# Kernel optimization log

Measured on AMD Instinct MI355X. Metric: run time of the kernel, lower is better.

Reference implementation:

```python
import jax, jax.numpy as jnp
import numpy as np

N_NODES = 50000
N_EDGES = 1600000
IN_DIM, HID_DIM, OUT_DIM = 512, 256, 128
N_IDX = 8192


def _graph_conv(x, src, dst, W, b, n_nodes):
    # DGL GraphConv, norm='both': D_dst^{-1/2} A D_src^{-1/2} x W + b
    ones = jnp.ones(src.shape[0], dtype=x.dtype)
    deg_out = jax.ops.segment_sum(ones, src, num_segments=n_nodes)
    deg_in = jax.ops.segment_sum(ones, dst, num_segments=n_nodes)
    ns = jax.lax.rsqrt(jnp.maximum(deg_out, 1.0))  # source norm
    nd = jax.lax.rsqrt(jnp.maximum(deg_in, 1.0))   # dest norm
    msg = (x * ns[:, None])[src]                   # gather [E, F]
    agg = jax.ops.segment_sum(msg, dst, num_segments=n_nodes)
    return (agg * nd[:, None]) @ W + b


def _gcn(x, src, dst, W1, b1, W2, b2, n_nodes):
    h = jax.nn.relu(_graph_conv(x, src, dst, W1, b1, n_nodes))
    return _graph_conv(h, src, dst, W2, b2, n_nodes)


def setup_inputs() -> dict:
    key = jax.random.key(0)
    ks = jax.random.split(key, 16)
    d = {
        'raw1': jax.random.normal(ks[0], (N_NODES, IN_DIM), jnp.float32),
        'raw2': jax.random.normal(ks[1], (N_NODES, IN_DIM), jnp.float32),
        'src1': jax.random.randint(ks[2], (N_EDGES,), 0, N_NODES),
        'dst1': jax.random.randint(ks[3], (N_EDGES,), 0, N_NODES),
        'src2': jax.random.randint(ks[4], (N_EDGES,), 0, N_NODES),
        'dst2': jax.random.randint(ks[5], (N_EDGES,), 0, N_NODES),
        'index': jax.random.randint(ks[6], (N_IDX,), 0, N_NODES),
    }
    def lin(k, fi, fo):
        s = 1.0 / np.sqrt(fi)
        return jax.random.uniform(k, (fi, fo), jnp.float32, -s, s)
    d['e1_W1'] = lin(ks[7], IN_DIM, HID_DIM); d['e1_b1'] = jnp.zeros(HID_DIM, jnp.float32)
    d['e1_W2'] = lin(ks[8], HID_DIM, OUT_DIM); d['e1_b2'] = jnp.zeros(OUT_DIM, jnp.float32)
    d['e2_W1'] = lin(ks[9], IN_DIM, HID_DIM); d['e2_b1'] = jnp.zeros(HID_DIM, jnp.float32)
    d['e2_W2'] = lin(ks[10], HID_DIM, OUT_DIM); d['e2_b2'] = jnp.zeros(OUT_DIM, jnp.float32)
    return d


def reference(raw1, raw2, src1, dst1, src2, dst2, index,
              e1_W1, e1_b1, e1_W2, e1_b2, e2_W1, e2_b1, e2_W2, e2_b2):
    n = raw1.shape[0]
    c1 = _gcn(raw1, src1, dst1, e1_W1, e1_b1, e1_W2, e1_b2, n)[index]
    c2 = _gcn(raw2, src2, dst2, e2_W1, e2_b1, e2_W2, e2_b2, n)[index]
    # F.normalize(dim=1), eps=1e-12
    c1 = c1 / jnp.maximum(jnp.linalg.norm(c1, axis=1, keepdims=True), 1e-12)
    c2 = c2 / jnp.maximum(jnp.linalg.norm(c2, axis=1, keepdims=True), 1e-12)
    z1 = c1 @ c1.T
    z2 = c2 @ c2.T
    z3 = c1 @ c2.T
    z3 = (z3 + z3.T) * 0.5
    z = (z1 + z2 + z3) * (1.0 / 3.0)
    return jnp.triu(z)
```

## Files before the change

kernel.cpp:

```cpp
#include <hip/hip_runtime.h>
#include <hip/hip_bf16.h>

using u16 = unsigned short;
using u32 = unsigned int;

typedef __attribute__((ext_vector_type(8))) short short8;
typedef __attribute__((ext_vector_type(4))) float f32x4;

__device__ __forceinline__ u16 f2bf_u16(float f) {
    __hip_bfloat16 h = __float2bfloat16(f);
    return __builtin_bit_cast(u16, h);
}
__device__ __forceinline__ float bfu(u32 u) { return __uint_as_float(u << 16); }

static constexpr int NN = 50000;
static constexpr int NE = 1600000;
static constexpr int NIDX = 8192;
static constexpr int NRANGE = 8;
static constexpr int RN = NN / NRANGE;
static constexpr int HCH = 16;
static constexpr int NK = NN * NRANGE;
static constexpr int SAB = (NK + 4095) / 4096;
static constexpr int CAPB = 262144;
static constexpr int PEB = 8192;
static constexpr int PGX = (NE + PEB - 1) / PEB;
static constexpr int CVB = 640;
static constexpr int PSTG = 1536;
static constexpr int ZLB = 64 * 63 / 2;
static constexpr int ZHB = ZLB / 2;
static constexpr int ZUB = 64 * 65 / 2;
static constexpr int AGB = NN / 4;
static constexpr int MT = (NN + 127) / 128;
static constexpr int SCX = 256;


__global__ __launch_bounds__(256)
void partition_kernel(const int* __restrict__ s1, const int* __restrict__ d1,
                      const int* __restrict__ s2, const int* __restrict__ d2,
                      int* __restrict__ bcur, u32* __restrict__ ebuf_d, u16* __restrict__ ebuf_s,
                      const float* __restrict__ W1a, const float* __restrict__ W1b,
                      const float* __restrict__ W2a, const float* __restrict__ W2b,
                      u16* __restrict__ W1t, u16* __restrict__ W2t) {
    if (blockIdx.x >= PGX) {
        int o = (blockIdx.x - PGX) + CVB * blockIdx.y;
        int idx = o * 256 + threadIdx.x;
        if (idx < 131072) {
            int k = idx >> 8, n = idx & 255;
            W1t[(size_t)n * 512 + k] = f2bf_u16(W1a[idx]);
        } else if (idx < 262144) {
            int j = idx - 131072;
            int k = j >> 8, n = j & 255;
            W1t[(size_t)131072 + (size_t)n * 512 + k] = f2bf_u16(W1b[j]);
        } else if (idx < 294912) {
            int j = idx - 262144;
            int k = j >> 7, n = j & 127;
            W2t[(size_t)n * 256 + k] = f2bf_u16(W2a[j]);
        } else if (idx < 327680) {
            int j = idx - 294912;
            int k = j >> 7, n = j & 127;
            W2t[(size_t)32768 + (size_t)n * 256 + k] = f2bf_u16(W2b[j]);
        }
        return;
    }
    __shared__ u32 stage_d[8][PSTG];
    __shared__ u16 stage_s[8][PSTG];
    __shared__ int cnt_d[8], cnt_s[8], base_d[8], base_s[8];
    int enc = blockIdx.y;
    const int* s = enc ? s2 : s1;
    const int* d = enc ? d2 : d1;
    if (threadIdx.x < 8) { cnt_d[threadIdx.x] = 0; cnt_s[threadIdx.x] = 0; }
    __syncthreads();
    int* bc_d = bcur + enc * 16;
    int* bc_s = bcur + enc * 16 + 8;
    u32* bd = ebuf_d + (size_t)enc * 8 * CAPB;
    u16* bs = ebuf_s + (size_t)enc * 8 * CAPB;
    int e0 = blockIdx.x * PEB;
    int e1 = min(e0 + PEB, NE);
    for (int e = e0 + threadIdx.x * 4; e < e1; e += 1024) {
        int4 sv = *(const int4*)(s + e);
        int4 dv = *(const int4*)(d + e);
        #pragma unroll
        for (int j = 0; j < 4; ++j) {
            int src = j == 0 ? sv.x : j == 1 ? sv.y : j == 2 ? sv.z : sv.w;
            int dst = j == 0 ? dv.x : j == 1 ? dv.y : j == 2 ? dv.z : dv.w;
            int rd = dst / RN;
            u32 entry = (u32)src | ((u32)(dst - rd * RN) << 16);
            int slot = atomicAdd(&cnt_d[rd], 1);
            if (slot < PSTG) stage_d[rd][slot] = entry;
            else { int gp = atomicAdd(&bc_d[rd], 1); bd[(size_t)rd * CAPB + gp] = entry; }
            int rs = src / RN;
            int slot2 = atomicAdd(&cnt_s[rs], 1);
            if (slot2 < PSTG) stage_s[rs][slot2] = (u16)(src - rs * RN);
            else { int gp = atomicAdd(&bc_s[rs], 1); bs[(size_t)rs * CAPB + gp] = (u16)(src - rs * RN); }
        }
    }
    __syncthreads();
    if (threadIdx.x < 8) {
        int b = threadIdx.x;
        base_d[b] = atomicAdd(&bc_d[b], min(cnt_d[b], PSTG));
        base_s[b] = atomicAdd(&bc_s[b], min(cnt_s[b], PSTG));
    }
    __syncthreads();
    #pragma unroll
    for (int b = 0; b < 8; ++b) {
        int nb = min(cnt_d[b], PSTG);
        for (int i = threadIdx.x; i < nb; i += 256)
            bd[(size_t)b * CAPB + base_d[b] + i] = stage_d[b][i];
        int ns = min(cnt_s[b], PSTG);
        for (int i = threadIdx.x; i < ns; i += 256)
            bs[(size_t)b * CAPB + base_s[b] + i] = stage_s[b][i];
    }
}


__global__ __launch_bounds__(256)
void bhist_kernel(const u32* __restrict__ ebuf_d, const u16* __restrict__ ebuf_s,
                  const int* __restrict__ bcur,
                  u32* __restrict__ partial2, u32* __restrict__ partial_out) {
    __shared__ u32 sh[RN * 2];
    int stripe = blockIdx.x & 7, chunk = blockIdx.x >> 3;
    int enc = blockIdx.y & 1, type = blockIdx.y >> 1;
    if (type == 0) {
        for (int i = threadIdx.x; i < RN * 2; i += 256) sh[i] = 0;
        __syncthreads();
        int size = bcur[enc * 16 + stripe];
        int cs = (size + HCH - 1) / HCH;
        int lo = chunk * cs, hi = min(lo + cs, size);
        const u32* b = ebuf_d + ((size_t)enc * 8 + stripe) * CAPB;
        for (int i = lo + threadIdx.x; i < hi; i += 256) {
            u32 e = b[i];
            u32 idx = (e >> 16) * 8 + (e & 0xffffu) / RN;
            atomicAdd(&sh[idx >> 2], 1u << ((idx & 3) * 8));
        }
        __syncthreads();
        u32* p2 = partial2 + ((size_t)enc * HCH + chunk) * (NN * 2) + stripe * (RN * 2);
        for (int i = threadIdx.x; i < RN * 2; i += 256) p2[i] = sh[i];
    } else {
        for (int i = threadIdx.x; i < RN / 2; i += 256) sh[i] = 0;
        __syncthreads();
        int size = bcur[enc * 16 + 8 + stripe];
        int cs = (size + HCH - 1) / HCH;
        int lo = chunk * cs, hi = min(lo + cs, size);
        const u16* b = ebuf_s + ((size_t)enc * 8 + stripe) * CAPB;
        for (int i = lo + threadIdx.x; i < hi; i += 256) {
            u32 sl = b[i];
            atomicAdd(&sh[sl >> 1], 1u << ((sl & 1) * 16));
        }
        __syncthreads();
        u32* po = partial_out + ((size_t)enc * HCH + chunk) * (NN / 2) + stripe * (RN / 2);
        for (int i = threadIdx.x; i < RN / 2; i += 256) po[i] = sh[i];
    }
}

__global__ void reduce_hist_kernel(const u32* __restrict__ partial2,
                                   const u32* __restrict__ partial_out,
                                   int* __restrict__ deg2, float* __restrict__ norms) {
    int i = blockIdx.x * blockDim.x + threadIdx.x;
    if (i >= 2 * NN) return;
    int enc = i / NN;
    int dst = i - enc * NN;
    int cnt[8];
    #pragma unroll
    for (int r = 0; r < 8; ++r) cnt[r] = 0;
    for (int c = 0; c < HCH; ++c) {
        const u32* p = partial2 + ((size_t)enc * HCH + c) * (NN * 2) + dst * 2;
        u32 w0 = p[0], w1 = p[1];
        cnt[0] += w0 & 0xff; cnt[1] += (w0 >> 8) & 0xff; cnt[2] += (w0 >> 16) & 0xff; cnt[3] += w0 >> 24;
        cnt[4] += w1 & 0xff; cnt[5] += (w1 >> 8) & 0xff; cnt[6] += (w1 >> 16) & 0xff; cnt[7] += w1 >> 24;
    }
    int* dp = deg2 + (size_t)enc * NK + dst * 8;
    int din = 0;
    #pragma unroll
    for (int r = 0; r < 8; ++r) { dp[r] = cnt[r]; din += cnt[r]; }
    norms[(enc * 2 + 1) * NN + dst] = rsqrtf(fmaxf((float)din, 1.f));
    int dout = 0;
    for (int c = 0; c < HCH; ++c) {
        u32 w = partial_out[((size_t)enc * HCH + c) * (NN / 2) + (dst >> 1)];
        dout += (w >> ((dst & 1) * 16)) & 0xffff;
    }
    norms[(enc * 2 + 0) * NN + dst] = rsqrtf(fmaxf((float)dout, 1.f));
}


__global__ __launch_bounds__(1024)
void scanA_kernel(const int* __restrict__ deg2, int* __restrict__ rp2_all, int* __restrict__ tot) {
    int enc = blockIdx.y;
    const int* deg = deg2 + (size_t)enc * NK;
    int* rp = rp2_all + (size_t)enc * (NK + 1);
    __shared__ int wsum[16];
    int t = threadIdx.x, lane = t & 63, wid = t >> 6;
    int i0 = blockIdx.x * 4096 + t * 4;
    int4 v = make_int4(0, 0, 0, 0);
    bool in = (i0 + 3 < NK);
    if (in) v = *(const int4*)(deg + i0);
    int s = v.x + v.y + v.z + v.w;
    int x = s;
    #pragma unroll
    for (int d = 1; d < 64; d <<= 1) {
        int y = __shfl_up(x, d, 64);
        if (lane >= d) x += y;
    }
    if (lane == 63) wsum[wid] = x;
    __syncthreads();
    if (t == 0) {
        int run = 0;
        #pragma unroll
        for (int w = 0; w < 16; ++w) { int q = wsum[w]; wsum[w] = run; run += q; }
        tot[enc * SAB + blockIdx.x] = run;
    }
    __syncthreads();
    if (in) {
        int excl = wsum[wid] + x - s;
        rp[i0] = excl;
        rp[i0 + 1] = excl + v.x;
        rp[i0 + 2] = excl + v.x + v.y;
        rp[i0 + 3] = excl + v.x + v.y + v.z;
    }
}

__global__ __launch_bounds__(256)
void scanC_kernel(int* __restrict__ rp2_all, int* __restrict__ cur2_all, const int* __restrict__ tot) {
    int enc = blockIdx.y;
    int* rp = rp2_all + (size_t)enc * (NK + 1);
    int* cur = cur2_all + (size_t)enc * NK;
    int nA = blockIdx.x >> 2;
    int part = 0;
    for (int i = threadIdx.x; i < nA; i += 256) part += tot[enc * SAB + i];
    #pragma unroll
    for (int d = 1; d < 64; d <<= 1) part += __shfl_xor(part, d, 64);
    __shared__ int red[4];
    __shared__ int soff;
    int lane = threadIdx.x & 63, wv = threadIdx.x >> 6;
    if (lane == 0) red[wv] = part;
    __syncthreads();
    if (threadIdx.x == 0) soff = red[0] + red[1] + red[2] + red[3];
    __syncthreads();
    int off = soff;
    int idx = (blockIdx.x * 256 + threadIdx.x) * 4;
    if (idx < NK) {
        int4 v = *(const int4*)(rp + idx);
        v.x += off; v.y += off; v.z += off; v.w += off;
        *(int4*)(rp + idx) = v;
        *(int4*)(cur + idx) = v;
    }
    if (blockIdx.x == 0 && threadIdx.x == 0) rp[NK] = NE;
}


__device__ __forceinline__ void scatter_body(const u32* __restrict__ ebuf_d,
                                             const int* __restrict__ bcur,
                                             int* __restrict__ cur2_all, u16* __restrict__ csr_all,
                                             int stripe, int chunk, int enc) {
    int size = bcur[enc * 16 + stripe];
    int cs = (size + 63) / 64;
    int lo = chunk * cs, hi = min(lo + cs, size);
    const u32* b = ebuf_d + ((size_t)enc * 8 + stripe) * CAPB;
    int* cursor = cur2_all + (size_t)enc * NK;
    u16* csr = csr_all + (size_t)enc * NE;
    int base = stripe * RN;
    for (int i = lo + threadIdx.x; i < hi; i += 256) {
        u32 e = b[i];
        int src = e & 0xffff;
        int dst = base + (int)(e >> 16);
        int key = dst * 8 + src / RN;
        int pos = atomicAdd(&cursor[key], 1);
        csr[pos] = (u16)src;
    }
}


template<bool A_F32, bool OUT_BF16, bool TRIANG, bool SCALE>
__device__ __forceinline__ void gemm_device(const void* __restrict__ A_, const u16* __restrict__ Bt,
                                            void* __restrict__ C_, const float* __restrict__ rowscale,
                                            int M, int N, int K, int it, int jt, u16* smem) {
    int t = threadIdx.x;
    int brow = it * 128, bcol = jt * 128;
    float* Cf = (float*)C_;
    u16* As = smem;
    u16* Bs = smem + 128 * 40;
    int lane = t & 63, wv = t >> 6;
    int wr = wv >> 1, wc = wv & 1;
    f32x4 acc[4][4];
    #pragma unroll
    for (int m = 0; m < 4; ++m)
        #pragma unroll
        for (int n = 0; n < 4; ++n) acc[m][n] = f32x4{0.f, 0.f, 0.f, 0.f};

    float4 a_f0[4], a_f1[4];
    uint4  a_h0[2], a_h1[2];
    uint4  b_h0[2], b_h1[2];

#define LOADT(S, kk) do {                                                          \
    if constexpr (A_F32) {                                                         \
        const float* A = (const float*)A_;                                         \
        _Pragma("unroll")                                                          \
        for (int p = 0; p < 4; ++p) {                                              \
            int r = p * 32 + (t >> 3), c = (t & 7) * 4;                            \
            int gr = brow + r;                                                     \
            a_f##S[p] = make_float4(0.f, 0.f, 0.f, 0.f);                           \
            if (gr < M) a_f##S[p] = *(const float4*)(A + (size_t)gr * K + (kk) + c); \
        }                                                                          \
    } else {                                                                       \
        const u16* A = (const u16*)A_;                                             \
        _Pragma("unroll")                                                          \
        for (int p = 0; p < 2; ++p) {                                              \
            int r = p * 64 + (t >> 2), c = (t & 3) * 8;                            \
            int gr = brow + r;                                                     \
            a_h##S[p] = make_uint4(0u, 0u, 0u, 0u);                                \
            if (gr < M) a_h##S[p] = *(const uint4*)(A + (size_t)gr * K + (kk) + c); \
        }                                                                          \
    }                                                                              \
    _Pragma("unroll")                                                              \
    for (int p = 0; p < 2; ++p) {                                                  \
        int r = p * 64 + (t >> 2), c = (t & 3) * 8;                                \
        int gn = bcol + r;                                                         \
        b_h##S[p] = make_uint4(0u, 0u, 0u, 0u);                                    \
        if (gn < N) b_h##S[p] = *(const uint4*)(Bt + (size_t)gn * K + (kk) + c);   \
    }                                                                              \
} while (0)

#define STORET(S) do {                                                             \
    if constexpr (A_F32) {                                                         \
        _Pragma("unroll")                                                          \
        for (int p = 0; p < 4; ++p) {                                              \
            int r = p * 32 + (t >> 3), c = (t & 7) * 4;                            \
            u32 lo = (u32)f2bf_u16(a_f##S[p].x) | ((u32)f2bf_u16(a_f##S[p].y) << 16); \
            u32 hi = (u32)f2bf_u16(a_f##S[p].z) | ((u32)f2bf_u16(a_f##S[p].w) << 16); \
            *(uint2*)&As[r * 40 + c] = make_uint2(lo, hi);                         \
        }                                                                          \
    } else {                                                                       \
        _Pragma("unroll")                                                          \
        for (int p = 0; p < 2; ++p) {                                              \
            int r = p * 64 + (t >> 2), c = (t & 3) * 8;                            \
            *(uint4*)&As[r * 40 + c] = a_h##S[p];                                  \
        }                                                                          \
    }                                                                              \
    _Pragma("unroll")                                                              \
    for (int p = 0; p < 2; ++p) {                                                  \
        int r = p * 64 + (t >> 2), c = (t & 3) * 8;                                \
        *(uint4*)&Bs[r * 40 + c] = b_h##S[p];                                      \
    }                                                                              \
} while (0)

    auto compute = [&]() {
        int kg = (lane >> 4) * 8;
        short8 av[4], bv[4];
        #pragma unroll
        for (int m = 0; m < 4; ++m)
            av[m] = *(const short8*)&As[(wr * 64 + m * 16 + (lane & 15)) * 40 + kg];
        #pragma unroll
        for (int n = 0; n < 4; ++n)
            bv[n] = *(const short8*)&Bs[(wc * 64 + n * 16 + (lane & 15)) * 40 + kg];
        #pragma unroll
        for (int m = 0; m < 4; ++m)
            #pragma unroll
            for (int n = 0; n < 4; ++n)
                acc[m][n] = __builtin_amdgcn_mfma_f32_16x16x32_bf16(av[m], bv[n], acc[m][n], 0, 0, 0);
    };

    LOADT(0, 0);
    LOADT(1, 32);
    for (int k0 = 0; k0 < K; k0 += 64) {
        STORET(0);
        __syncthreads();
        if (k0 + 64 < K) LOADT(0, k0 + 64);
        compute();
        __syncthreads();
        STORET(1);
        __syncthreads();
        if (k0 + 96 < K) LOADT(1, k0 + 96);
        compute();
        __syncthreads();
    }
#undef LOADT
#undef STORET

    const int lane15 = lane & 15, lanehi = lane >> 4;
    if (OUT_BF16) {
        u16* stg = smem + wv * 1024;
        #pragma unroll
        for (int m = 0; m < 4; ++m) {
            #pragma unroll
            for (int n = 0; n < 4; ++n)
                #pragma unroll
                for (int r = 0; r < 4; ++r) {
                    float v = acc[m][n][r];
                    if (SCALE) v *= rowscale[brow + wr * 64 + m * 16 + lanehi * 4 + r];
                    stg[(lanehi * 4 + r) * 64 + n * 16 + lane15] = f2bf_u16(v);
                }
            #pragma unroll
            for (int pass = 0; pass < 2; ++pass) {
                int lr = pass * 8 + (lane >> 3);
                int grow = brow + wr * 64 + m * 16 + lr;
                uint4 w = *(uint4*)&stg[lr * 64 + (lane & 7) * 8];
                if (grow < M)
                    *(uint4*)((u16*)C_ + (size_t)grow * N + bcol + wc * 64 + (lane & 7) * 8) = w;
            }
        }
    } else {
        float* stg = (float*)smem + wv * 1024;
        #pragma unroll
        for (int m = 0; m < 4; ++m) {
            #pragma unroll
            for (int n = 0; n < 4; ++n)
                #pragma unroll
                for (int r = 0; r < 4; ++r) {
                    int row = brow + wr * 64 + m * 16 + lanehi * 4 + r;
                    int col = bcol + wc * 64 + n * 16 + lane15;
                    float v = acc[m][n][r];
                    if (SCALE) v *= rowscale[row];
                    if (TRIANG && col < row) v = 0.f;
                    stg[(lanehi * 4 + r) * 64 + n * 16 + lane15] = v;
                }
            #pragma unroll
            for (int pass = 0; pass < 4; ++pass) {
                int lr = pass * 4 + lanehi;
                int grow = brow + wr * 64 + m * 16 + lr;
                f32x4 w = *(f32x4*)&stg[lr * 64 + lane15 * 4];
                if (grow < M) {
                    float* dp = Cf + (size_t)grow * N + bcol + wc * 64 + lane15 * 4;
                    if (TRIANG) __builtin_nontemporal_store(w, (f32x4*)dp);
                    else *(f32x4*)dp = w;
                }
            }
        }
    }
}

__global__ __launch_bounds__(256)
void gemm1scat_kernel(const float* __restrict__ raw0, const float* __restrict__ raw1,
                      const u16* __restrict__ W1t, u16* __restrict__ Y1,
                      const float* __restrict__ norms,
                      const u32* __restrict__ ebuf_d, const int* __restrict__ bcur,
                      int* __restrict__ tick, int* __restrict__ cur2, u16* __restrict__ csr_all) {
    if (blockIdx.x >= MT) {
        u32 lin = blockIdx.x + gridDim.x * (blockIdx.y + gridDim.y * blockIdx.z);
        int stripe = lin & 7;
        __shared__ int tsh;
        if (threadIdx.x == 0) tsh = atomicAdd(&tick[stripe], 1);
        __syncthreads();
        int tkt = tsh;
        scatter_body(ebuf_d, bcur, cur2, csr_all, stripe, tkt & 63, tkt >> 6);
        return;
    }
    __shared__ alignas(16) u16 smem[128 * 40 * 2];
    int enc = blockIdx.z;
    gemm_device<true, true, false, true>(
        enc ? raw1 : raw0, W1t + (size_t)enc * 512 * 256,
        Y1 + (size_t)enc * NN * 256, norms + (size_t)2 * enc * NN,
        NN, 256, 512, blockIdx.x, blockIdx.y, smem);
}

__global__ __launch_bounds__(256)
void gemm2_kernel(const u16* __restrict__ H1, const u16* __restrict__ W2t,
                  u16* __restrict__ Y2, const float* __restrict__ norms) {
    __shared__ alignas(16) u16 smem[128 * 40 * 2];
    int enc = blockIdx.z;
    gemm_device<false, true, false, true>(
        H1 + (size_t)enc * NN * 256, W2t + (size_t)enc * 256 * 128,
        Y2 + (size_t)enc * NN * 128, norms + (size_t)2 * enc * NN,
        NN, 128, 256, blockIdx.x, 0, smem);
}

__global__ __launch_bounds__(256)
void zgemm_kernel(const u16* __restrict__ R, float* __restrict__ out) {
    int b = blockIdx.x;
    int i = (int)((129.0f - sqrtf(129.f * 129.f - 8.f * b)) * 0.5f);
    while ((i + 1) * (129 - (i + 1)) / 2 <= b) ++i;
    while (i * (129 - i) / 2 > b) --i;
    int it = i;
    int jt = i + (b - i * (129 - i) / 2);
    __shared__ alignas(16) u16 smem[128 * 40 * 2];
    gemm_device<false, false, true, false>(R, R, out, nullptr, NIDX, NIDX, 256, it, jt, smem);
}


template<int F, bool RELU, bool OUT_BF16, bool ZFILL>
__global__ __launch_bounds__(256)
void agg_kernel(const u16* __restrict__ Yall, const int* __restrict__ rp2_all,
                const u16* __restrict__ csr_all, const float* __restrict__ norms,
                const float* __restrict__ bias0, const float* __restrict__ bias1,
                void* __restrict__ out_all, float* __restrict__ zout) {
    constexpr int VPL = F / 64;
    int enc = blockIdx.y;
    int bid = blockIdx.x;
    if (ZFILL) {
        if (bid < ZHB) {
            int b = enc * ZHB + bid;
            float fit = (sqrtf(8.f * b + 1.f) + 1.f) * 0.5f;
            int it = (int)fit;
            if (it * (it - 1) / 2 > b) --it;
            else if ((it + 1) * it / 2 <= b) ++it;
            int jt = b - it * (it - 1) / 2;
            int brow = it * 128, bcol = jt * 128;
            f32x4 z = {0.f, 0.f, 0.f, 0.f};
            #pragma unroll
            for (int pq = 0; pq < 16; ++pq) {
                int idx = pq * 256 + threadIdx.x;
                int r = idx >> 5, c4 = idx & 31;
                __builtin_nontemporal_store(z, (f32x4*)(zout + (size_t)(brow + r) * NIDX + bcol + c4 * 4));
            }
            return;
        }
        bid -= ZHB;
    }
    const u16* Y = Yall + (size_t)enc * NN * F;
    const int* rp2 = rp2_all + (size_t)enc * (NK + 1);
    const u16* csr = csr_all + (size_t)enc * NE;
    const float* nd = norms + (size_t)(2 * enc + 1) * NN;
    const float* bias = enc ? bias1 : bias0;
    int lane = threadIdx.x & 63;
    int node = bid * 4 + (threadIdx.x >> 6);
    int e0 = rp2[node * 8], e1 = rp2[node * 8 + 8];
    float acc[VPL];
    #pragma unroll
    for (int j = 0; j < VPL; ++j) acc[j] = 0.f;
    const int off = lane * VPL;

    int e = e0;
    for (; e < e1 && (e & 7) != 0; ++e) {
        int s = csr[e];
        if (VPL == 4) {
            uint2 d = *(const uint2*)(Y + (size_t)s * F + off);
            acc[0] += bfu(d.x & 0xffffu); acc[1] += bfu(d.x >> 16);
            acc[2] += bfu(d.y & 0xffffu); acc[3] += bfu(d.y >> 16);
        } else {
            u32 d = *(const u32*)(Y + (size_t)s * F + off);
            acc[0] += bfu(d & 0xffffu); acc[1] += bfu(d >> 16);
        }
    }
    if (VPL == 4) {
        for (; e + 16 <= e1; e += 16) {
            uint4 ia = *(const uint4*)(csr + e);
            uint4 ib = *(const uint4*)(csr + e + 8);
            int s0 = ia.x & 0xffff, s1 = ia.x >> 16, s2 = ia.y & 0xffff, s3 = ia.y >> 16;
            int s4 = ia.z & 0xffff, s5 = ia.z >> 16, s6 = ia.w & 0xffff, s7 = ia.w >> 16;
            int s8 = ib.x & 0xffff, s9 = ib.x >> 16, sa = ib.y & 0xffff, sb = ib.y >> 16;
            int sc = ib.z & 0xffff, sd = ib.z >> 16, se = ib.w & 0xffff, sf = ib.w >> 16;
            uint2 d0 = *(const uint2*)(Y + (size_t)s0 * F + off);
            uint2 d1 = *(const uint2*)(Y + (size_t)s1 * F + off);
            uint2 d2 = *(const uint2*)(Y + (size_t)s2 * F + off);
            uint2 d3 = *(const uint2*)(Y + (size_t)s3 * F + off);
            uint2 d4 = *(const uint2*)(Y + (size_t)s4 * F + off);
            uint2 d5 = *(const uint2*)(Y + (size_t)s5 * F + off);
            uint2 d6 = *(const uint2*)(Y + (size_t)s6 * F + off);
            uint2 d7 = *(const uint2*)(Y + (size_t)s7 * F + off);
            uint2 d8 = *(const uint2*)(Y + (size_t)s8 * F + off);
            uint2 d9 = *(const uint2*)(Y + (size_t)s9 * F + off);
            uint2 da = *(const uint2*)(Y + (size_t)sa * F + off);
            uint2 db = *(const uint2*)(Y + (size_t)sb * F + off);
            uint2 dc = *(const uint2*)(Y + (size_t)sc * F + off);
            uint2 dd = *(const uint2*)(Y + (size_t)sd * F + off);
            uint2 de = *(const uint2*)(Y + (size_t)se * F + off);
            uint2 df = *(const uint2*)(Y + (size_t)sf * F + off);
            acc[0] += bfu(d0.x & 0xffffu); acc[1] += bfu(d0.x >> 16); acc[2] += bfu(d0.y & 0xffffu); acc[3] += bfu(d0.y >> 16);
            acc[0] += bfu(d1.x & 0xffffu); acc[1] += bfu(d1.x >> 16); acc[2] += bfu(d1.y & 0xffffu); acc[3] += bfu(d1.y >> 16);
            acc[0] += bfu(d2.x & 0xffffu); acc[1] += bfu(d2.x >> 16); acc[2] += bfu(d2.y & 0xffffu); acc[3] += bfu(d2.y >> 16);
            acc[0] += bfu(d3.x & 0xffffu); acc[1] += bfu(d3.x >> 16); acc[2] += bfu(d3.y & 0xffffu); acc[3] += bfu(d3.y >> 16);
            acc[0] += bfu(d4.x & 0xffffu); acc[1] += bfu(d4.x >> 16); acc[2] += bfu(d4.y & 0xffffu); acc[3] += bfu(d4.y >> 16);
            acc[0] += bfu(d5.x & 0xffffu); acc[1] += bfu(d5.x >> 16); acc[2] += bfu(d5.y & 0xffffu); acc[3] += bfu(d5.y >> 16);
            acc[0] += bfu(d6.x & 0xffffu); acc[1] += bfu(d6.x >> 16); acc[2] += bfu(d6.y & 0xffffu); acc[3] += bfu(d6.y >> 16);
            acc[0] += bfu(d7.x & 0xffffu); acc[1] += bfu(d7.x >> 16); acc[2] += bfu(d7.y & 0xffffu); acc[3] += bfu(d7.y >> 16);
            acc[0] += bfu(d8.x & 0xffffu); acc[1] += bfu(d8.x >> 16); acc[2] += bfu(d8.y & 0xffffu); acc[3] += bfu(d8.y >> 16);
            acc[0] += bfu(d9.x & 0xffffu); acc[1] += bfu(d9.x >> 16); acc[2] += bfu(d9.y & 0xffffu); acc[3] += bfu(d9.y >> 16);
            acc[0] += bfu(da.x & 0xffffu); acc[1] += bfu(da.x >> 16); acc[2] += bfu(da.y & 0xffffu); acc[3] += bfu(da.y >> 16);
            acc[0] += bfu(db.x & 0xffffu); acc[1] += bfu(db.x >> 16); acc[2] += bfu(db.y & 0xffffu); acc[3] += bfu(db.y >> 16);
            acc[0] += bfu(dc.x & 0xffffu); acc[1] += bfu(dc.x >> 16); acc[2] += bfu(dc.y & 0xffffu); acc[3] += bfu(dc.y >> 16);
            acc[0] += bfu(dd.x & 0xffffu); acc[1] += bfu(dd.x >> 16); acc[2] += bfu(dd.y & 0xffffu); acc[3] += bfu(dd.y >> 16);
            acc[0] += bfu(de.x & 0xffffu); acc[1] += bfu(de.x >> 16); acc[2] += bfu(de.y & 0xffffu); acc[3] += bfu(de.y >> 16);
            acc[0] += bfu(df.x & 0xffffu); acc[1] += bfu(df.x >> 16); acc[2] += bfu(df.y & 0xffffu); acc[3] += bfu(df.y >> 16);
        }
    }
    for (; e + 8 <= e1; e += 8) {
        uint4 iv = *(const uint4*)(csr + e);
        int s0 = iv.x & 0xffff, s1 = iv.x >> 16;
        int s2 = iv.y & 0xffff, s3 = iv.y >> 16;
        int s4 = iv.z & 0xffff, s5 = iv.z >> 16;
        int s6 = iv.w & 0xffff, s7 = iv.w >> 16;
        if (VPL == 4) {
            uint2 d0 = *(const uint2*)(Y + (size_t)s0 * F + off);
            uint2 d1 = *(const uint2*)(Y + (size_t)s1 * F + off);
            uint2 d2 = *(const uint2*)(Y + (size_t)s2 * F + off);
            uint2 d3 = *(const uint2*)(Y + (size_t)s3 * F + off);
            uint2 d4 = *(const uint2*)(Y + (size_t)s4 * F + off);
            uint2 d5 = *(const uint2*)(Y + (size_t)s5 * F + off);
            uint2 d6 = *(const uint2*)(Y + (size_t)s6 * F + off);
            uint2 d7 = *(const uint2*)(Y + (size_t)s7 * F + off);
            acc[0] += bfu(d0.x & 0xffffu); acc[1] += bfu(d0.x >> 16); acc[2] += bfu(d0.y & 0xffffu); acc[3] += bfu(d0.y >> 16);
            acc[0] += bfu(d1.x & 0xffffu); acc[1] += bfu(d1.x >> 16); acc[2] += bfu(d1.y & 0xffffu); acc[3] += bfu(d1.y >> 16);
            acc[0] += bfu(d2.x & 0xffffu); acc[1] += bfu(d2.x >> 16); acc[2] += bfu(d2.y & 0xffffu); acc[3] += bfu(d2.y >> 16);
            acc[0] += bfu(d3.x & 0xffffu); acc[1] += bfu(d3.x >> 16); acc[2] += bfu(d3.y & 0xffffu); acc[3] += bfu(d3.y >> 16);
            acc[0] += bfu(d4.x & 0xffffu); acc[1] += bfu(d4.x >> 16); acc[2] += bfu(d4.y & 0xffffu); acc[3] += bfu(d4.y >> 16);
            acc[0] += bfu(d5.x & 0xffffu); acc[1] += bfu(d5.x >> 16); acc[2] += bfu(d5.y & 0xffffu); acc[3] += bfu(d5.y >> 16);
            acc[0] += bfu(d6.x & 0xffffu); acc[1] += bfu(d6.x >> 16); acc[2] += bfu(d6.y & 0xffffu); acc[3] += bfu(d6.y >> 16);
            acc[0] += bfu(d7.x & 0xffffu); acc[1] += bfu(d7.x >> 16); acc[2] += bfu(d7.y & 0xffffu); acc[3] += bfu(d7.y >> 16);
        } else {
            u32 d0 = *(const u32*)(Y + (size_t)s0 * F + off);
            u32 d1 = *(const u32*)(Y + (size_t)s1 * F + off);
            u32 d2 = *(const u32*)(Y + (size_t)s2 * F + off);
            u32 d3 = *(const u32*)(Y + (size_t)s3 * F + off);
            u32 d4 = *(const u32*)(Y + (size_t)s4 * F + off);
            u32 d5 = *(const u32*)(Y + (size_t)s5 * F + off);
            u32 d6 = *(const u32*)(Y + (size_t)s6 * F + off);
            u32 d7 = *(const u32*)(Y + (size_t)s7 * F + off);
            acc[0] += bfu(d0 & 0xffffu); acc[1] += bfu(d0 >> 16);
            acc[0] += bfu(d1 & 0xffffu); acc[1] += bfu(d1 >> 16);
            acc[0] += bfu(d2 & 0xffffu); acc[1] += bfu(d2 >> 16);
            acc[0] += bfu(d3 & 0xffffu); acc[1] += bfu(d3 >> 16);
            acc[0] += bfu(d4 & 0xffffu); acc[1] += bfu(d4 >> 16);
            acc[0] += bfu(d5 & 0xffffu); acc[1] += bfu(d5 >> 16);
            acc[0] += bfu(d6 & 0xffffu); acc[1] += bfu(d6 >> 16);
            acc[0] += bfu(d7 & 0xffffu); acc[1] += bfu(d7 >> 16);
        }
    }
    for (; e < e1; ++e) {
        int s = csr[e];
        if (VPL == 4) {
            uint2 d = *(const uint2*)(Y + (size_t)s * F + off);
            acc[0] += bfu(d.x & 0xffffu); acc[1] += bfu(d.x >> 16);
            acc[2] += bfu(d.y & 0xffffu); acc[3] += bfu(d.y >> 16);
        } else {
            u32 d = *(const u32*)(Y + (size_t)s * F + off);
            acc[0] += bfu(d & 0xffffu); acc[1] += bfu(d >> 16);
        }
    }

    float ndv = nd[node];
    #pragma unroll
    for (int j = 0; j < VPL; ++j) {
        float o = acc[j] * ndv + bias[off + j];
        if (RELU) o = fmaxf(o, 0.f);
        if (OUT_BF16) ((u16*)out_all)[(size_t)enc * NN * F + (size_t)node * F + off + j] = f2bf_u16(o);
        else ((float*)out_all)[(size_t)enc * NN * F + (size_t)node * F + off + j] = o;
    }
}


__global__ __launch_bounds__(256)
void build_r_kernel(const float* __restrict__ H2a, const float* __restrict__ H2b,
                    const int* __restrict__ index, u16* __restrict__ R) {
    int lane = threadIdx.x & 63;
    int row = blockIdx.x * 4 + (threadIdx.x >> 6);
    int g = index[row];
    float2 a = *(const float2*)(H2a + (size_t)g * 128 + lane * 2);
    float2 b = *(const float2*)(H2b + (size_t)g * 128 + lane * 2);
    float sa = a.x * a.x + a.y * a.y;
    float sb = b.x * b.x + b.y * b.y;
    #pragma unroll
    for (int d = 1; d < 64; d <<= 1) {
        sa += __shfl_xor(sa, d, 64);
        sb += __shfl_xor(sb, d, 64);
    }
    float inva = 1.f / fmaxf(sqrtf(sa), 1e-12f);
    float invb = 1.f / fmaxf(sqrtf(sb), 1e-12f);
    float ax = a.x * inva, ay = a.y * inva;
    float bx = b.x * invb, by = b.y * invb;
    const float c2 = 0.5f, c3 = 0.28867513459481287f;
    u16* Rp = R + (size_t)row * 256;
    Rp[lane * 2]           = f2bf_u16((ax + bx) * c2);
    Rp[lane * 2 + 1]       = f2bf_u16((ay + by) * c2);
    Rp[128 + lane * 2]     = f2bf_u16((ax - bx) * c3);
    Rp[128 + lane * 2 + 1] = f2bf_u16((ay - by) * c3);
}


extern "C" void kernel_launch(void* const* d_in, const int* in_sizes, int n_in,
                              void* d_out, int out_size, void* d_ws, size_t ws_size,
                              hipStream_t stream) {
    (void)in_sizes; (void)n_in; (void)out_size; (void)ws_size;
    const float* raw0 = (const float*)d_in[0];
    const float* raw1 = (const float*)d_in[1];
    const int* src1 = (const int*)d_in[2], *dst1 = (const int*)d_in[3];
    const int* src2 = (const int*)d_in[4], *dst2 = (const int*)d_in[5];
    const int* index = (const int*)d_in[6];
    const float* W1a = (const float*)d_in[7];  const float* b1a = (const float*)d_in[8];
    const float* W2a = (const float*)d_in[9];  const float* b2a = (const float*)d_in[10];
    const float* W1b = (const float*)d_in[11]; const float* b1b = (const float*)d_in[12];
    const float* W2b = (const float*)d_in[13]; const float* b2b = (const float*)d_in[14];

    char* wp = (char*)d_ws;
    auto alloc = [&](size_t bytes) -> char* {
        char* r = wp;
        wp += (bytes + 255) & ~(size_t)255;
        return r;
    };
    float* norms   = (float*)alloc((size_t)4 * NN * 4);
    int*   deg2    = (int*)alloc((size_t)2 * NK * 4);
    int*   rp2     = (int*)alloc((size_t)2 * (NK + 1) * 4);
    int*   cur2    = (int*)alloc((size_t)2 * NK * 4);
    int*   tot     = (int*)alloc((size_t)2 * SAB * 4);
    int*   bcur    = (int*)alloc(48 * 4);
    u16*   csr_all = (u16*)alloc((size_t)2 * NE * 2);
    u16*   W1t     = (u16*)alloc((size_t)2 * 512 * 256 * 2);
    u16*   W2t     = (u16*)alloc((size_t)2 * 256 * 128 * 2);
    u16*   Y1      = (u16*)alloc((size_t)2 * NN * 256 * 2);
    u16*   H1      = (u16*)alloc((size_t)2 * NN * 256 * 2);
    u16*   Y2      = (u16*)alloc((size_t)2 * NN * 128 * 2);
    float* H2      = (float*)alloc((size_t)2 * NN * 128 * 4);
    u16*   R       = (u16*)alloc((size_t)NIDX * 256 * 2);
    int*   tick    = bcur + 32;
    u32* partial2    = (u32*)Y1;
    u32* partial_out = (u32*)H1;
    u32* ebuf_d      = (u32*)Y2;
    u16* ebuf_s      = (u16*)H2;

    hipMemsetAsync(bcur, 0, 48 * 4, stream);
    partition_kernel<<<dim3(PGX + CVB, 2), 256, 0, stream>>>(
        src1, dst1, src2, dst2, bcur, ebuf_d, ebuf_s, W1a, W1b, W2a, W2b, W1t, W2t);
    bhist_kernel<<<dim3(8 * HCH, 4), 256, 0, stream>>>(ebuf_d, ebuf_s, bcur, partial2, partial_out);
    reduce_hist_kernel<<<(2 * NN + 255) / 256, 256, 0, stream>>>(partial2, partial_out, deg2, norms);
    scanA_kernel<<<dim3(SAB, 2), 1024, 0, stream>>>(deg2, rp2, tot);
    scanC_kernel<<<dim3((NK / 4 + 255) / 256, 2), 256, 0, stream>>>(rp2, cur2, tot);

    gemm1scat_kernel<<<dim3(MT + SCX, 2, 2), 256, 0, stream>>>(
        raw0, raw1, W1t, Y1, norms, ebuf_d, bcur, tick, cur2, csr_all);
    agg_kernel<256, true, true, true><<<dim3(ZHB + AGB, 2), 256, 0, stream>>>(
        Y1, rp2, csr_all, norms, b1a, b1b, H1, (float*)d_out);
    gemm2_kernel<<<dim3(MT, 1, 2), 256, 0, stream>>>(H1, W2t, Y2, norms);
    agg_kernel<128, false, false, false><<<dim3(AGB, 2), 256, 0, stream>>>(
        Y2, rp2, csr_all, norms, b2a, b2b, H2, nullptr);

    build_r_kernel<<<NIDX / 4, 256, 0, stream>>>(H2, H2 + (size_t)NN * 128, index, R);
    zgemm_kernel<<<dim3(ZUB, 1, 1), 256, 0, stream>>>(R, (float*)d_out);
}
```

Before: 624.0 us.

## Aggregate second GCN layer only at indexed nodes, fused with normalization

The full second-layer aggregation over all 50k nodes for both encoders is replaced by a kernel that aggregates only the 8192 rows selected by index. The same kernel then applies bias and L2 normalization and builds the combined bf16 R matrix. This removes most of the layer-2 gather traffic and the write and reread of H2. The general agg_kernel is simplified to its VPL==4, bf16-output path. Duplicate indices now repeat their aggregation work, and the gather runs with fewer waves.

```diff
diff --git a/kernel.cpp b/kernel.cpp
--- a/kernel.cpp
+++ b/kernel.cpp
@@ -520,56 +520,49 @@
     int e = e0;
     for (; e < e1 && (e & 7) != 0; ++e) {
         int s = csr[e];
-        if (VPL == 4) {
-            uint2 d = *(const uint2*)(Y + (size_t)s * F + off);
-            acc[0] += bfu(d.x & 0xffffu); acc[1] += bfu(d.x >> 16);
-            acc[2] += bfu(d.y & 0xffffu); acc[3] += bfu(d.y >> 16);
-        } else {
-            u32 d = *(const u32*)(Y + (size_t)s * F + off);
-            acc[0] += bfu(d & 0xffffu); acc[1] += bfu(d >> 16);
-        }
-    }
-    if (VPL == 4) {
-        for (; e + 16 <= e1; e += 16) {
-            uint4 ia = *(const uint4*)(csr + e);
-            uint4 ib = *(const uint4*)(csr + e + 8);
-            int s0 = ia.x & 0xffff, s1 = ia.x >> 16, s2 = ia.y & 0xffff, s3 = ia.y >> 16;
-            int s4 = ia.z & 0xffff, s5 = ia.z >> 16, s6 = ia.w & 0xffff, s7 = ia.w >> 16;
-            int s8 = ib.x & 0xffff, s9 = ib.x >> 16, sa = ib.y & 0xffff, sb = ib.y >> 16;
-            int sc = ib.z & 0xffff, sd = ib.z >> 16, se = ib.w & 0xffff, sf = ib.w >> 16;
-            uint2 d0 = *(const uint2*)(Y + (size_t)s0 * F + off);
-            uint2 d1 = *(const uint2*)(Y + (size_t)s1 * F + off);
-            uint2 d2 = *(const uint2*)(Y + (size_t)s2 * F + off);
-            uint2 d3 = *(const uint2*)(Y + (size_t)s3 * F + off);
-            uint2 d4 = *(const uint2*)(Y + (size_t)s4 * F + off);
-            uint2 d5 = *(const uint2*)(Y + (size_t)s5 * F + off);
-            uint2 d6 = *(const uint2*)(Y + (size_t)s6 * F + off);
-            uint2 d7 = *(const uint2*)(Y + (size_t)s7 * F + off);
-            uint2 d8 = *(const uint2*)(Y + (size_t)s8 * F + off);
-            uint2 d9 = *(const uint2*)(Y + (size_t)s9 * F + off);
-            uint2 da = *(const uint2*)(Y + (size_t)sa * F + off);
-            uint2 db = *(const uint2*)(Y + (size_t)sb * F + off);
-            uint2 dc = *(const uint2*)(Y + (size_t)sc * F + off);
-            uint2 dd = *(const uint2*)(Y + (size_t)sd * F + off);
-            uint2 de = *(const uint2*)(Y + (size_t)se * F + off);
-            uint2 df = *(const uint2*)(Y + (size_t)sf * F + off);
-            acc[0] += bfu(d0.x & 0xffffu); acc[1] += bfu(d0.x >> 16); acc[2] += bfu(d0.y & 0xffffu); acc[3] += bfu(d0.y >> 16);
-            acc[0] += bfu(d1.x & 0xffffu); acc[1] += bfu(d1.x >> 16); acc[2] += bfu(d1.y & 0xffffu); acc[3] += bfu(d1.y >> 16);
-            acc[0] += bfu(d2.x & 0xffffu); acc[1] += bfu(d2.x >> 16); acc[2] += bfu(d2.y & 0xffffu); acc[3] += bfu(d2.y >> 16);
-            acc[0] += bfu(d3.x & 0xffffu); acc[1] += bfu(d3.x >> 16); acc[2] += bfu(d3.y & 0xffffu); acc[3] += bfu(d3.y >> 16);
-            acc[0] += bfu(d4.x & 0xffffu); acc[1] += bfu(d4.x >> 16); acc[2] += bfu(d4.y & 0xffffu); acc[3] += bfu(d4.y >> 16);
-            acc[0] += bfu(d5.x & 0xffffu); acc[1] += bfu(d5.x >> 16); acc[2] += bfu(d5.y & 0xffffu); acc[3] += bfu(d5.y >> 16);
-            acc[0] += bfu(d6.x & 0xffffu); acc[1] += bfu(d6.x >> 16); acc[2] += bfu(d6.y & 0xffffu); acc[3] += bfu(d6.y >> 16);
-            acc[0] += bfu(d7.x & 0xffffu); acc[1] += bfu(d7.x >> 16); acc[2] += bfu(d7.y & 0xffffu); acc[3] += bfu(d7.y >> 16);
-            acc[0] += bfu(d8.x & 0xffffu); acc[1] += bfu(d8.x >> 16); acc[2] += bfu(d8.y & 0xffffu); acc[3] += bfu(d8.y >> 16);
-            acc[0] += bfu(d9.x & 0xffffu); acc[1] += bfu(d9.x >> 16); acc[2] += bfu(d9.y & 0xffffu); acc[3] += bfu(d9.y >> 16);
-            acc[0] += bfu(da.x & 0xffffu); acc[1] += bfu(da.x >> 16); acc[2] += bfu(da.y & 0xffffu); acc[3] += bfu(da.y >> 16);
-            acc[0] += bfu(db.x & 0xffffu); acc[1] += bfu(db.x >> 16); acc[2] += bfu(db.y & 0xffffu); acc[3] += bfu(db.y >> 16);
-            acc[0] += bfu(dc.x & 0xffffu); acc[1] += bfu(dc.x >> 16); acc[2] += bfu(dc.y & 0xffffu); acc[3] += bfu(dc.y >> 16);
-            acc[0] += bfu(dd.x & 0xffffu); acc[1] += bfu(dd.x >> 16); acc[2] += bfu(dd.y & 0xffffu); acc[3] += bfu(dd.y >> 16);
-            acc[0] += bfu(de.x & 0xffffu); acc[1] += bfu(de.x >> 16); acc[2] += bfu(de.y & 0xffffu); acc[3] += bfu(de.y >> 16);
-            acc[0] += bfu(df.x & 0xffffu); acc[1] += bfu(df.x >> 16); acc[2] += bfu(df.y & 0xffffu); acc[3] += bfu(df.y >> 16);
-        }
+        uint2 d = *(const uint2*)(Y + (size_t)s * F + off);
+        acc[0] += bfu(d.x & 0xffffu); acc[1] += bfu(d.x >> 16);
+        acc[2] += bfu(d.y & 0xffffu); acc[3] += bfu(d.y >> 16);
+    }
+    for (; e + 16 <= e1; e += 16) {
+        uint4 ia = *(const uint4*)(csr + e);
+        uint4 ib = *(const uint4*)(csr + e + 8);
+        int s0 = ia.x & 0xffff, s1 = ia.x >> 16, s2 = ia.y & 0xffff, s3 = ia.y >> 16;
+        int s4 = ia.z & 0xffff, s5 = ia.z >> 16, s6 = ia.w & 0xffff, s7 = ia.w >> 16;
+        int s8 = ib.x & 0xffff, s9 = ib.x >> 16, sa = ib.y & 0xffff, sb = ib.y >> 16;
+        int sc = ib.z & 0xffff, sd = ib.z >> 16, se = ib.w & 0xffff, sf = ib.w >> 16;
+        uint2 d0 = *(const uint2*)(Y + (size_t)s0 * F + off);
+        uint2 d1 = *(const uint2*)(Y + (size_t)s1 * F + off);
+        uint2 d2 = *(const uint2*)(Y + (size_t)s2 * F + off);
+        uint2 d3 = *(const uint2*)(Y + (size_t)s3 * F + off);
+        uint2 d4 = *(const uint2*)(Y + (size_t)s4 * F + off);
+        uint2 d5 = *(const uint2*)(Y + (size_t)s5 * F + off);
+        uint2 d6 = *(const uint2*)(Y + (size_t)s6 * F + off);
+        uint2 d7 = *(const uint2*)(Y + (size_t)s7 * F + off);
+        uint2 d8 = *(const uint2*)(Y + (size_t)s8 * F + off);
+        uint2 d9 = *(const uint2*)(Y + (size_t)s9 * F + off);
+        uint2 da = *(const uint2*)(Y + (size_t)sa * F + off);
+        uint2 db = *(const uint2*)(Y + (size_t)sb * F + off);
+        uint2 dc = *(const uint2*)(Y + (size_t)sc * F + off);
+        uint2 dd = *(const uint2*)(Y + (size_t)sd * F + off);
+        uint2 de = *(const uint2*)(Y + (size_t)se * F + off);
+        uint2 df = *(const uint2*)(Y + (size_t)sf * F + off);
+        acc[0] += bfu(d0.x & 0xffffu); acc[1] += bfu(d0.x >> 16); acc[2] += bfu(d0.y & 0xffffu); acc[3] += bfu(d0.y >> 16);
+        acc[0] += bfu(d1.x & 0xffffu); acc[1] += bfu(d1.x >> 16); acc[2] += bfu(d1.y & 0xffffu); acc[3] += bfu(d1.y >> 16);
+        acc[0] += bfu(d2.x & 0xffffu); acc[1] += bfu(d2.x >> 16); acc[2] += bfu(d2.y & 0xffffu); acc[3] += bfu(d2.y >> 16);
+        acc[0] += bfu(d3.x & 0xffffu); acc[1] += bfu(d3.x >> 16); acc[2] += bfu(d3.y & 0xffffu); acc[3] += bfu(d3.y >> 16);
+        acc[0] += bfu(d4.x & 0xffffu); acc[1] += bfu(d4.x >> 16); acc[2] += bfu(d4.y & 0xffffu); acc[3] += bfu(d4.y >> 16);
+        acc[0] += bfu(d5.x & 0xffffu); acc[1] += bfu(d5.x >> 16); acc[2] += bfu(d5.y & 0xffffu); acc[3] += bfu(d5.y >> 16);
+        acc[0] += bfu(d6.x & 0xffffu); acc[1] += bfu(d6.x >> 16); acc[2] += bfu(d6.y & 0xffffu); acc[3] += bfu(d6.y >> 16);
+        acc[0] += bfu(d7.x & 0xffffu); acc[1] += bfu(d7.x >> 16); acc[2] += bfu(d7.y & 0xffffu); acc[3] += bfu(d7.y >> 16);
+        acc[0] += bfu(d8.x & 0xffffu); acc[1] += bfu(d8.x >> 16); acc[2] += bfu(d8.y & 0xffffu); acc[3] += bfu(d8.y >> 16);
+        acc[0] += bfu(d9.x & 0xffffu); acc[1] += bfu(d9.x >> 16); acc[2] += bfu(d9.y & 0xffffu); acc[3] += bfu(d9.y >> 16);
+        acc[0] += bfu(da.x & 0xffffu); acc[1] += bfu(da.x >> 16); acc[2] += bfu(da.y & 0xffffu); acc[3] += bfu(da.y >> 16);
+        acc[0] += bfu(db.x & 0xffffu); acc[1] += bfu(db.x >> 16); acc[2] += bfu(db.y & 0xffffu); acc[3] += bfu(db.y >> 16);
+        acc[0] += bfu(dc.x & 0xffffu); acc[1] += bfu(dc.x >> 16); acc[2] += bfu(dc.y & 0xffffu); acc[3] += bfu(dc.y >> 16);
+        acc[0] += bfu(dd.x & 0xffffu); acc[1] += bfu(dd.x >> 16); acc[2] += bfu(dd.y & 0xffffu); acc[3] += bfu(dd.y >> 16);
+        acc[0] += bfu(de.x & 0xffffu); acc[1] += bfu(de.x >> 16); acc[2] += bfu(de.y & 0xffffu); acc[3] += bfu(de.y >> 16);
+        acc[0] += bfu(df.x & 0xffffu); acc[1] += bfu(df.x >> 16); acc[2] += bfu(df.y & 0xffffu); acc[3] += bfu(df.y >> 16);
     }
     for (; e + 8 <= e1; e += 8) {
         uint4 iv = *(const uint4*)(csr + e);
@@ -577,52 +570,28 @@
         int s2 = iv.y & 0xffff, s3 = iv.y >> 16;
         int s4 = iv.z & 0xffff, s5 = iv.z >> 16;
         int s6 = iv.w & 0xffff, s7 = iv.w >> 16;
-        if (VPL == 4) {
-            uint2 d0 = *(const uint2*)(Y + (size_t)s0 * F + off);
-            uint2 d1 = *(const uint2*)(Y + (size_t)s1 * F + off);
-            uint2 d2 = *(const uint2*)(Y + (size_t)s2 * F + off);
-            uint2 d3 = *(const uint2*)(Y + (size_t)s3 * F + off);
-            uint2 d4 = *(const uint2*)(Y + (size_t)s4 * F + off);
-            uint2 d5 = *(const uint2*)(Y + (size_t)s5 * F + off);
-            uint2 d6 = *(const uint2*)(Y + (size_t)s6 * F + off);
-            uint2 d7 = *(const uint2*)(Y + (size_t)s7 * F + off);
-            acc[0] += bfu(d0.x & 0xffffu); acc[1] += bfu(d0.x >> 16); acc[2] += bfu(d0.y & 0xffffu); acc[3] += bfu(d0.y >> 16);
-            acc[0] += bfu(d1.x & 0xffffu); acc[1] += bfu(d1.x >> 16); acc[2] += bfu(d1.y & 0xffffu); acc[3] += bfu(d1.y >> 16);
-            acc[0] += bfu(d2.x & 0xffffu); acc[1] += bfu(d2.x >> 16); acc[2] += bfu(d2.y & 0xffffu); acc[3] += bfu(d2.y >> 16);
-            acc[0] += bfu(d3.x & 0xffffu); acc[1] += bfu(d3.x >> 16); acc[2] += bfu(d3.y & 0xffffu); acc[3] += bfu(d3.y >> 16);
-            acc[0] += bfu(d4.x & 0xffffu); acc[1] += bfu(d4.x >> 16); acc[2] += bfu(d4.y & 0xffffu); acc[3] += bfu(d4.y >> 16);
-            acc[0] += bfu(d5.x & 0xffffu); acc[1] += bfu(d5.x >> 16); acc[2] += bfu(d5.y & 0xffffu); acc[3] += bfu(d5.y >> 16);
-            acc[0] += bfu(d6.x & 0xffffu); acc[1] += bfu(d6.x >> 16); acc[2] += bfu(d6.y & 0xffffu); acc[3] += bfu(d6.y >> 16);
-            acc[0] += bfu(d7.x & 0xffffu); acc[1] += bfu(d7.x >> 16); acc[2] += bfu(d7.y & 0xffffu); acc[3] += bfu(d7.y >> 16);
-        } else {
-            u32 d0 = *(const u32*)(Y + (size_t)s0 * F + off);
-            u32 d1 = *(const u32*)(Y + (size_t)s1 * F + off);
-            u32 d2 = *(const u32*)(Y + (size_t)s2 * F + off);
-            u32 d3 = *(const u32*)(Y + (size_t)s3 * F + off);
-            u32 d4 = *(const u32*)(Y + (size_t)s4 * F + off);
-            u32 d5 = *(const u32*)(Y + (size_t)s5 * F + off);
-            u32 d6 = *(const u32*)(Y + (size_t)s6 * F + off);
-            u32 d7 = *(const u32*)(Y + (size_t)s7 * F + off);
-            acc[0] += bfu(d0 & 0xffffu); acc[1] += bfu(d0 >> 16);
-            acc[0] += bfu(d1 & 0xffffu); acc[1] += bfu(d1 >> 16);
-            acc[0] += bfu(d2 & 0xffffu); acc[1] += bfu(d2 >> 16);
-            acc[0] += bfu(d3 & 0xffffu); acc[1] += bfu(d3 >> 16);
-            acc[0] += bfu(d4 & 0xffffu); acc[1] += bfu(d4 >> 16);
-            acc[0] += bfu(d5 & 0xffffu); acc[1] += bfu(d5 >> 16);
-            acc[0] += bfu(d6 & 0xffffu); acc[1] += bfu(d6 >> 16);
-            acc[0] += bfu(d7 & 0xffffu); acc[1] += bfu(d7 >> 16);
-        }
+        uint2 d0 = *(const uint2*)(Y + (size_t)s0 * F + off);
+        uint2 d1 = *(const uint2*)(Y + (size_t)s1 * F + off);
+        uint2 d2 = *(const uint2*)(Y + (size_t)s2 * F + off);
+        uint2 d3 = *(const uint2*)(Y + (size_t)s3 * F + off);
+        uint2 d4 = *(const uint2*)(Y + (size_t)s4 * F + off);
+        uint2 d5 = *(const uint2*)(Y + (size_t)s5 * F + off);
+        uint2 d6 = *(const uint2*)(Y + (size_t)s6 * F + off);
+        uint2 d7 = *(const uint2*)(Y + (size_t)s7 * F + off);
+        acc[0] += bfu(d0.x & 0xffffu); acc[1] += bfu(d0.x >> 16); acc[2] += bfu(d0.y & 0xffffu); acc[3] += bfu(d0.y >> 16);
+        acc[0] += bfu(d1.x & 0xffffu); acc[1] += bfu(d1.x >> 16); acc[2] += bfu(d1.y & 0xffffu); acc[3] += bfu(d1.y >> 16);
+        acc[0] += bfu(d2.x & 0xffffu); acc[1] += bfu(d2.x >> 16); acc[2] += bfu(d2.y & 0xffffu); acc[3] += bfu(d2.y >> 16);
+        acc[0] += bfu(d3.x & 0xffffu); acc[1] += bfu(d3.x >> 16); acc[2] += bfu(d3.y & 0xffffu); acc[3] += bfu(d3.y >> 16);
+        acc[0] += bfu(d4.x & 0xffffu); acc[1] += bfu(d4.x >> 16); acc[2] += bfu(d4.y & 0xffffu); acc[3] += bfu(d4.y >> 16);
+        acc[0] += bfu(d5.x & 0xffffu); acc[1] += bfu(d5.x >> 16); acc[2] += bfu(d5.y & 0xffffu); acc[3] += bfu(d5.y >> 16);
+        acc[0] += bfu(d6.x & 0xffffu); acc[1] += bfu(d6.x >> 16); acc[2] += bfu(d6.y & 0xffffu); acc[3] += bfu(d6.y >> 16);
+        acc[0] += bfu(d7.x & 0xffffu); acc[1] += bfu(d7.x >> 16); acc[2] += bfu(d7.y & 0xffffu); acc[3] += bfu(d7.y >> 16);
     }
     for (; e < e1; ++e) {
         int s = csr[e];
-        if (VPL == 4) {
-            uint2 d = *(const uint2*)(Y + (size_t)s * F + off);
-            acc[0] += bfu(d.x & 0xffffu); acc[1] += bfu(d.x >> 16);
-            acc[2] += bfu(d.y & 0xffffu); acc[3] += bfu(d.y >> 16);
-        } else {
-            u32 d = *(const u32*)(Y + (size_t)s * F + off);
-            acc[0] += bfu(d & 0xffffu); acc[1] += bfu(d >> 16);
-        }
+        uint2 d = *(const uint2*)(Y + (size_t)s * F + off);
+        acc[0] += bfu(d.x & 0xffffu); acc[1] += bfu(d.x >> 16);
+        acc[2] += bfu(d.y & 0xffffu); acc[3] += bfu(d.y >> 16);
     }
 
     float ndv = nd[node];
@@ -630,37 +599,79 @@
     for (int j = 0; j < VPL; ++j) {
         float o = acc[j] * ndv + bias[off + j];
         if (RELU) o = fmaxf(o, 0.f);
-        if (OUT_BF16) ((u16*)out_all)[(size_t)enc * NN * F + (size_t)node * F + off + j] = f2bf_u16(o);
-        else ((float*)out_all)[(size_t)enc * NN * F + (size_t)node * F + off + j] = o;
+        ((u16*)out_all)[(size_t)enc * NN * F + (size_t)node * F + off + j] = f2bf_u16(o);
     }
 }
 
 
 __global__ __launch_bounds__(256)
-void build_r_kernel(const float* __restrict__ H2a, const float* __restrict__ H2b,
-                    const int* __restrict__ index, u16* __restrict__ R) {
+void aggr_kernel(const u16* __restrict__ Y2all, const int* __restrict__ rp2_all,
+                 const u16* __restrict__ csr_all, const float* __restrict__ norms,
+                 const float* __restrict__ b2a, const float* __restrict__ b2b,
+                 const int* __restrict__ index, u16* __restrict__ R) {
+    int pos = blockIdx.x * 4 + (threadIdx.x >> 6);
     int lane = threadIdx.x & 63;
-    int row = blockIdx.x * 4 + (threadIdx.x >> 6);
-    int g = index[row];
-    float2 a = *(const float2*)(H2a + (size_t)g * 128 + lane * 2);
-    float2 b = *(const float2*)(H2b + (size_t)g * 128 + lane * 2);
-    float sa = a.x * a.x + a.y * a.y;
-    float sb = b.x * b.x + b.y * b.y;
-    #pragma unroll
-    for (int d = 1; d < 64; d <<= 1) {
-        sa += __shfl_xor(sa, d, 64);
-        sb += __shfl_xor(sb, d, 64);
-    }
-    float inva = 1.f / fmaxf(sqrtf(sa), 1e-12f);
-    float invb = 1.f / fmaxf(sqrtf(sb), 1e-12f);
-    float ax = a.x * inva, ay = a.y * inva;
-    float bx = b.x * invb, by = b.y * invb;
+    int node = index[pos];
+    const int off = lane * 2;
+    float cx[2], cy[2];
+    #pragma unroll
+    for (int enc = 0; enc < 2; ++enc) {
+        const u16* Y = Y2all + (size_t)enc * NN * 128;
+        const int* rp2 = rp2_all + (size_t)enc * (NK + 1);
+        const u16* csr = csr_all + (size_t)enc * NE;
+        int e0 = rp2[node * 8], e1 = rp2[node * 8 + 8];
+        float a0 = 0.f, a1 = 0.f;
+        int e = e0;
+        for (; e < e1 && (e & 7) != 0; ++e) {
+            int s = csr[e];
+            u32 d = *(const u32*)(Y + (size_t)s * 128 + off);
+            a0 += bfu(d & 0xffffu); a1 += bfu(d >> 16);
+        }
+        for (; e + 8 <= e1; e += 8) {
+            uint4 iv = *(const uint4*)(csr + e);
+            int s0 = iv.x & 0xffff, s1 = iv.x >> 16;
+            int s2 = iv.y & 0xffff, s3 = iv.y >> 16;
+            int s4 = iv.z & 0xffff, s5 = iv.z >> 16;
+            int s6 = iv.w & 0xffff, s7 = iv.w >> 16;
+            u32 d0 = *(const u32*)(Y + (size_t)s0 * 128 + off);
+            u32 d1 = *(const u32*)(Y + (size_t)s1 * 128 + off);
+            u32 d2 = *(const u32*)(Y + (size_t)s2 * 128 + off);
+            u32 d3 = *(const u32*)(Y + (size_t)s3 * 128 + off);
+            u32 d4 = *(const u32*)(Y + (size_t)s4 * 128 + off);
+            u32 d5 = *(const u32*)(Y + (size_t)s5 * 128 + off);
+            u32 d6 = *(const u32*)(Y + (size_t)s6 * 128 + off);
+            u32 d7 = *(const u32*)(Y + (size_t)s7 * 128 + off);
+            a0 += bfu(d0 & 0xffffu); a1 += bfu(d0 >> 16);
+            a0 += bfu(d1 & 0xffffu); a1 += bfu(d1 >> 16);
+            a0 += bfu(d2 & 0xffffu); a1 += bfu(d2 >> 16);
+            a0 += bfu(d3 & 0xffffu); a1 += bfu(d3 >> 16);
+            a0 += bfu(d4 & 0xffffu); a1 += bfu(d4 >> 16);
+            a0 += bfu(d5 & 0xffffu); a1 += bfu(d5 >> 16);
+            a0 += bfu(d6 & 0xffffu); a1 += bfu(d6 >> 16);
+            a0 += bfu(d7 & 0xffffu); a1 += bfu(d7 >> 16);
+        }
+        for (; e < e1; ++e) {
+            int s = csr[e];
+            u32 d = *(const u32*)(Y + (size_t)s * 128 + off);
+            a0 += bfu(d & 0xffffu); a1 += bfu(d >> 16);
+        }
+        float ndv = norms[(2 * enc + 1) * NN + node];
+        const float* bias = enc ? b2b : b2a;
+        float o0 = a0 * ndv + bias[off];
+        float o1 = a1 * ndv + bias[off + 1];
+        float ss = o0 * o0 + o1 * o1;
+        #pragma unroll
+        for (int dshf = 1; dshf < 64; dshf <<= 1) ss += __shfl_xor(ss, dshf, 64);
+        float inv = 1.f / fmaxf(sqrtf(ss), 1e-12f);
+        cx[enc] = o0 * inv;
+        cy[enc] = o1 * inv;
+    }
     const float c2 = 0.5f, c3 = 0.28867513459481287f;
-    u16* Rp = R + (size_t)row * 256;
-    Rp[lane * 2]           = f2bf_u16((ax + bx) * c2);
-    Rp[lane * 2 + 1]       = f2bf_u16((ay + by) * c2);
-    Rp[128 + lane * 2]     = f2bf_u16((ax - bx) * c3);
-    Rp[128 + lane * 2 + 1] = f2bf_u16((ay - by) * c3);
+    u16* Rp = R + (size_t)pos * 256;
+    u32 w0 = (u32)f2bf_u16((cx[0] + cx[1]) * c2) | ((u32)f2bf_u16((cy[0] + cy[1]) * c2) << 16);
+    u32 w1 = (u32)f2bf_u16((cx[0] - cx[1]) * c3) | ((u32)f2bf_u16((cy[0] - cy[1]) * c3) << 16);
+    *(u32*)(Rp + off) = w0;
+    *(u32*)(Rp + 128 + off) = w1;
 }
 
 
@@ -717,9 +728,6 @@
     agg_kernel<256, true, true, true><<<dim3(ZHB + AGB, 2), 256, 0, stream>>>(
         Y1, rp2, csr_all, norms, b1a, b1b, H1, (float*)d_out);
     gemm2_kernel<<<dim3(MT, 1, 2), 256, 0, stream>>>(H1, W2t, Y2, norms);
-    agg_kernel<128, false, false, false><<<dim3(AGB, 2), 256, 0, stream>>>(
-        Y2, rp2, csr_all, norms, b2a, b2b, H2, nullptr);
-
-    build_r_kernel<<<NIDX / 4, 256, 0, stream>>>(H2, H2 + (size_t)NN * 128, index, R);
+    aggr_kernel<<<NIDX / 4, 256, 0, stream>>>(Y2, rp2, csr_all, norms, b2a, b2b, index, R);
     zgemm_kernel<<<dim3(ZUB, 1, 1), 256, 0, stream>>>(R, (float*)d_out);
 }
```

Result: faster. 528.6 us (median of 2 runs) (-15.3%).
